# Kernel tuning notes

Hardware: AMD Instinct MI355X
Metric: run time of the kernel (lower is better)

The kernel has to match this reference:

```python
import jax, jax.numpy as jnp
import numpy as np

DIM = 1024; N_LAYERS = 4; N_HEADS = 16; HEAD_DIM = DIM // N_HEADS
HIDDEN = 2816; VOCAB = 256; EPS = 1e-5; THETA = 10000.0
B, S = 1, 2048


def _rmsnorm(x, w):
    xf = x.astype(jnp.float32)
    n = xf * jax.lax.rsqrt(jnp.mean(xf * xf, axis=-1, keepdims=True) + EPS)
    return n.astype(x.dtype) * w


def _rope(x, cos, sin):
    # x: [B,S,H,hd]; torch view_as_complex pairs consecutive elements (0,1),(2,3),...
    xr = x[..., 0::2].astype(jnp.float32)
    xi = x[..., 1::2].astype(jnp.float32)
    c = cos[None, :, None, :]
    s = sin[None, :, None, :]
    outr = xr * c - xi * s
    outi = xr * s + xi * c
    out = jnp.stack([outr, outi], axis=-1).reshape(x.shape)
    return out.astype(x.dtype)


def setup_inputs() -> dict:
    key = jax.random.key(0)
    ks = jax.random.split(key, 10)
    std = 0.02
    def w(k, shape):
        return jax.random.normal(k, shape, jnp.float32) * std
    return {
        "tokens": jax.random.randint(ks[0], (B, S), 0, VOCAB, dtype=jnp.int32),
        "tok_emb": w(ks[1], (VOCAB, DIM)),
        "wq": w(ks[2], (N_LAYERS, DIM, DIM)),
        "wk": w(ks[3], (N_LAYERS, DIM, DIM)),
        "wv": w(ks[4], (N_LAYERS, DIM, DIM)),
        "wo": w(ks[5], (N_LAYERS, DIM, DIM)),
        "w1": w(ks[6], (N_LAYERS, HIDDEN, DIM)),
        "w2": w(ks[7], (N_LAYERS, DIM, HIDDEN)),
        "w3": w(ks[8], (N_LAYERS, HIDDEN, DIM)),
        "attn_norm_w": jnp.ones((N_LAYERS, DIM), jnp.float32),
        "ffn_norm_w": jnp.ones((N_LAYERS, DIM), jnp.float32),
        "final_norm_w": jnp.ones((DIM,), jnp.float32),
        "out_w": w(ks[9], (VOCAB, DIM)),
    }


def reference(tokens, tok_emb, wq, wk, wv, wo, w1, w2, w3,
              attn_norm_w, ffn_norm_w, final_norm_w, out_w):
    seqlen = tokens.shape[1]
    # precompute_freqs_cis
    inv = 1.0 / (THETA ** (jnp.arange(0, HEAD_DIM, 2, dtype=jnp.float32) / HEAD_DIM))
    t = jnp.arange(seqlen, dtype=jnp.float32)
    freqs = jnp.outer(t, inv)          # [S, hd/2]
    cos, sin = jnp.cos(freqs), jnp.sin(freqs)
    scale = 1.0 / np.sqrt(HEAD_DIM)

    h = tok_emb[tokens]                # [B,S,D]

    def block(h, p):
        lwq, lwk, lwv, lwo, lw1, lw2, lw3, anw, fnw = p
        x = _rmsnorm(h, anw)
        q = (x @ lwq.T).reshape(B, seqlen, N_HEADS, HEAD_DIM)
        k = (x @ lwk.T).reshape(B, seqlen, N_HEADS, HEAD_DIM)
        v = (x @ lwv.T).reshape(B, seqlen, N_HEADS, HEAD_DIM)
        q = _rope(q, cos, sin)
        k = _rope(k, cos, sin)
        # non-causal full attention (eval mode: no diffusion mask, no dropout)
        scores = jnp.einsum('bqhd,bkhd->bhqk', q, k) * scale
        probs = jax.nn.softmax(scores, axis=-1)
        attn = jnp.einsum('bhqk,bkhd->bqhd', probs, v).reshape(B, seqlen, DIM)
        h = h + attn @ lwo.T
        x = _rmsnorm(h, fnw)
        ff = (jax.nn.silu(x @ lw1.T) * (x @ lw3.T)) @ lw2.T
        return h + ff, None

    h, _ = jax.lax.scan(block, h, (wq, wk, wv, wo, w1, w2, w3, attn_norm_w, ffn_norm_w))
    h = _rmsnorm(h, final_norm_w)
    # targets=None path: logits only for the last position
    return h[:, -1:, :] @ out_w.T      # [B,1,VOCAB]
```

## Files before the change

kernel.cpp:

```cpp
#include <hip/hip_runtime.h>
#include <stdint.h>

typedef __bf16 bf16;
typedef __bf16 bf16x4 __attribute__((ext_vector_type(4)));
typedef __bf16 bf16x8 __attribute__((ext_vector_type(8)));
typedef float f32x4 __attribute__((ext_vector_type(4)));
typedef float f32x16 __attribute__((ext_vector_type(16)));

#define SEQ 2048
#define DIM 1024
#define NHEAD 16
#define HDIM 64
#define HID 2816
#define NLAYER 4

__device__ __forceinline__ void gload_lds16(const void* g, void* l) {
  __builtin_amdgcn_global_load_lds(
      (const __attribute__((address_space(1))) void*)g,
      (__attribute__((address_space(3))) void*)l, 16, 0, 0);
}

template <int MODE, int BM, int BN>
__global__ __launch_bounds__(256) void gemm_bt(
    const bf16* __restrict__ A, const bf16* __restrict__ B,
    bf16* __restrict__ Cb, float* __restrict__ Cf, const float* R,
    int M, int N, int K)
{
  constexpr int MR = BM / 32;
  constexpr int NR = BN / 32;
  constexpr int LA = BM / 64;
  constexpr int LB = BN / 64;
  __shared__ bf16 As[2 * BM * 32];
  __shared__ bf16 Bs[2 * BN * 32];
  const int tid  = threadIdx.x;
  const int wv   = tid >> 6;
  const int lane = tid & 63;
  const int lo = lane & 15, hi = lane >> 4;
  const int row0 = blockIdx.y * BM;
  const int col0 = blockIdx.x * BN;
  const int wr = (wv >> 1) * (BM / 2);
  const int wc = (wv & 1) * (BN / 2);

  f32x4 acc[MR][NR];
  const f32x4 zero = {0.f, 0.f, 0.f, 0.f};
#pragma unroll
  for (int m = 0; m < MR; ++m)
#pragma unroll
    for (int n = 0; n < NR; ++n) acc[m][n] = zero;

  const bf16* ag = A + (size_t)(row0 + (tid >> 2)) * K + (tid & 3) * 8;
  const bf16* bg = B + (size_t)(col0 + (tid >> 2)) * K + (tid & 3) * 8;

  auto stage = [&](int buf, int k) {
#pragma unroll
    for (int i = 0; i < LA; ++i)
      gload_lds16(ag + k + (size_t)i*64*K, &As[buf*BM*32 + i*2048 + wv*512]);
#pragma unroll
    for (int i = 0; i < LB; ++i)
      gload_lds16(bg + k + (size_t)i*64*K, &Bs[buf*BN*32 + i*2048 + wv*512]);
  };
  auto compute = [&](int buf) {
    bf16x8 af[MR], bfv[NR];
#pragma unroll
    for (int m = 0; m < MR; ++m)
      af[m] = *(const bf16x8*)&As[buf*BM*32 + (wr + m*16 + lo)*32 + hi*8];
#pragma unroll
    for (int n = 0; n < NR; ++n)
      bfv[n] = *(const bf16x8*)&Bs[buf*BN*32 + (wc + n*16 + lo)*32 + hi*8];
#pragma unroll
    for (int m = 0; m < MR; ++m)
#pragma unroll
      for (int n = 0; n < NR; ++n)
        acc[m][n] = __builtin_amdgcn_mfma_f32_16x16x32_bf16(af[m], bfv[n], acc[m][n], 0, 0, 0);
  };

  stage(0, 0);
  __syncthreads();
  for (int k0 = 0; k0 < K; k0 += 64) {
    stage(1, k0 + 32);
    compute(0);
    __syncthreads();
    if (k0 + 64 < K) stage(0, k0 + 64);
    compute(1);
    __syncthreads();
  }

#pragma unroll
  for (int m = 0; m < MR; ++m)
#pragma unroll
    for (int n = 0; n < NR; ++n)
#pragma unroll
      for (int r = 0; r < 4; ++r) {
        const int row = row0 + wr + m * 16 + hi * 4 + r;
        const int col = col0 + wc + n * 16 + lo;
        const size_t idx = (size_t)row * N + col;
        if (MODE == 0) Cb[idx] = (bf16)acc[m][n][r];
        else           Cf[idx] = R[idx] + acc[m][n][r];
      }
}

__device__ __forceinline__ void softmax_pv(
    f32x16& s, float& m, float& lsum, f32x16& o0, f32x16& o1,
    const bf16x8 (&vf)[2][2], int h)
{
  float mx = s[0];
#pragma unroll
  for (int r = 1; r < 16; ++r) mx = fmaxf(mx, s[r]);
  mx = fmaxf(mx, __shfl_xor(mx, 32));
  if (!__all(mx <= m + 8.0f)) {
    float mnew = fmaxf(m, mx);
    float corr = __expf(m - mnew);
    m = mnew; lsum *= corr;
#pragma unroll
    for (int r = 0; r < 16; ++r) { o0[r] *= corr; o1[r] *= corr; }
  }
  float p[16]; float ps = 0.f;
#pragma unroll
  for (int r = 0; r < 16; ++r) { p[r] = __expf(s[r] - m); ps += p[r]; }
  ps += __shfl_xor(ps, 32);
  lsum += ps;

  unsigned int w[4][2];
#pragma unroll
  for (int g = 0; g < 4; ++g)
#pragma unroll
    for (int t2 = 0; t2 < 2; ++t2) {
      union { bf16 b[2]; unsigned int u; } pk;
      pk.b[0] = (bf16)p[g*4 + 2*t2];
      pk.b[1] = (bf16)p[g*4 + 2*t2 + 1];
      w[g][t2] = pk.u;
    }

#pragma unroll
  for (int c = 0; c < 2; ++c) {
    unsigned int keep0 = h ? w[2*c+1][0] : w[2*c][0];
    unsigned int keep1 = h ? w[2*c+1][1] : w[2*c][1];
    unsigned int send0 = h ? w[2*c][0]   : w[2*c+1][0];
    unsigned int send1 = h ? w[2*c][1]   : w[2*c+1][1];
    unsigned int r0 = __shfl_xor(send0, 32);
    unsigned int r1 = __shfl_xor(send1, 32);
    union { unsigned int u[4]; bf16x8 v; } pf;
    pf.u[0] = h ? r0 : keep0;
    pf.u[1] = h ? r1 : keep1;
    pf.u[2] = h ? keep0 : r0;
    pf.u[3] = h ? keep1 : r1;
    __builtin_amdgcn_s_setprio(1);
    o0 = __builtin_amdgcn_mfma_f32_32x32x16_bf16(vf[c][0], pf.v, o0, 0, 0, 0);
    o1 = __builtin_amdgcn_mfma_f32_32x32x16_bf16(vf[c][1], pf.v, o1, 0, 0, 0);
    __builtin_amdgcn_s_setprio(0);
  }
}

__device__ __forceinline__ void attn_tile64(
    const bf16* __restrict__ kb, const bf16* __restrict__ vb,
    const bf16x8 (&qfA)[4], const bf16x8 (&qfB)[4],
    bf16x8 (&kc)[4], bf16x8 (&kn)[4],
    f32x16& oA0, f32x16& oA1, f32x16& oB0, f32x16& oB1,
    float& mA, float& lA, float& mB, float& lB,
    int j0, int jn, int q5, int h)
{
  bf16x8 vf[2][2];
#pragma unroll
  for (int c = 0; c < 2; ++c)
#pragma unroll
    for (int dh = 0; dh < 2; ++dh)
      vf[c][dh] = *(const bf16x8*)&vb[(size_t)(dh*32 + q5)*2048 + j0 + c*16];
  {
    const bf16* kp = kb + (size_t)(jn + q5)*3072;
#pragma unroll
    for (int dc = 0; dc < 4; ++dc) kn[dc] = *(const bf16x8*)(kp + dc*16);
  }
  f32x16 sA, sB;
#pragma unroll
  for (int r = 0; r < 16; ++r) { sA[r] = 0.f; sB[r] = 0.f; }
  __builtin_amdgcn_s_setprio(1);
#pragma unroll
  for (int dc = 0; dc < 4; ++dc) {
    sA = __builtin_amdgcn_mfma_f32_32x32x16_bf16(kc[dc], qfA[dc], sA, 0, 0, 0);
    sB = __builtin_amdgcn_mfma_f32_32x32x16_bf16(kc[dc], qfB[dc], sB, 0, 0, 0);
  }
  __builtin_amdgcn_s_setprio(0);

  softmax_pv(sA, mA, lA, oA0, oA1, vf, h);
  softmax_pv(sB, mB, lB, oB0, oB1, vf, h);
}

__global__ __launch_bounds__(256, 2) void attn_kernel(const bf16* __restrict__ qkv,
    const bf16* __restrict__ vt, bf16* __restrict__ outb)
{
  __shared__ float Osh[4][32][65];
  __shared__ float msh[4][32];
  __shared__ float lsh[4][32];

  const int tid = threadIdx.x;
  const int wv = tid >> 6;
  const int lane = tid & 63;
  const int q5 = lane & 31, h = lane >> 5;
  const int hh = blockIdx.x;
  const int q0 = blockIdx.y * 64;

  bf16x8 qfA[4], qfB[4];
#pragma unroll
  for (int dc = 0; dc < 4; ++dc) {
    bf16x8 xa = *(const bf16x8*)&qkv[(size_t)(q0 + q5)*3072      + hh*64 + h*8 + dc*16];
    bf16x8 xb = *(const bf16x8*)&qkv[(size_t)(q0 + 32 + q5)*3072 + hh*64 + h*8 + dc*16];
#pragma unroll
    for (int j = 0; j < 8; ++j) {
      xa[j] = (bf16)(0.125f * (float)xa[j]);
      xb[j] = (bf16)(0.125f * (float)xb[j]);
    }
    qfA[dc] = xa; qfB[dc] = xb;
  }

  const bf16* kb = qkv + 1024 + hh*64 + h*8;
  const bf16* vb = vt + (size_t)hh*64*2048 + h*8;

  f32x16 oA0, oA1, oB0, oB1;
#pragma unroll
  for (int r = 0; r < 16; ++r) { oA0[r]=0.f; oA1[r]=0.f; oB0[r]=0.f; oB1[r]=0.f; }
  float mA = -1e30f, lA = 0.f, mB = -1e30f, lB = 0.f;

  bf16x8 ka[4], ka2[4];
  {
    const bf16* kp = kb + (size_t)(wv*32 + q5)*3072;
#pragma unroll
    for (int dc = 0; dc < 4; ++dc) ka[dc] = *(const bf16x8*)(kp + dc*16);
  }

  for (int t = 0; t < 16; t += 2) {
    attn_tile64(kb, vb, qfA, qfB, ka, ka2, oA0, oA1, oB0, oB1,
                mA, lA, mB, lB,
                (wv + 4*t)*32,     ((wv + 4*(t+1)) & 63)*32, q5, h);
    attn_tile64(kb, vb, qfA, qfB, ka2, ka, oA0, oA1, oB0, oB1,
                mA, lA, mB, lB,
                (wv + 4*(t+1))*32, ((wv + 4*(t+2)) & 63)*32, q5, h);
  }

  const int q = tid >> 3, d0 = (tid & 7) * 8;
#pragma unroll
  for (int pass = 0; pass < 2; ++pass) {
    const f32x16& p0 = pass ? oB0 : oA0;
    const f32x16& p1 = pass ? oB1 : oA1;
#pragma unroll
    for (int r = 0; r < 16; ++r) {
      const int dr = (r & 3) + 8*(r >> 2) + 4*h;
      Osh[wv][q5][dr]      = p0[r];
      Osh[wv][q5][32 + dr] = p1[r];
    }
    if (h == 0) {
      msh[wv][q5] = pass ? mB : mA;
      lsh[wv][q5] = pass ? lB : lA;
    }
    __syncthreads();
    {
      float mm = fmaxf(fmaxf(msh[0][q], msh[1][q]), fmaxf(msh[2][q], msh[3][q]));
      float e0 = __expf(msh[0][q] - mm), e1 = __expf(msh[1][q] - mm),
            e2 = __expf(msh[2][q] - mm), e3 = __expf(msh[3][q] - mm);
      float L = e0*lsh[0][q] + e1*lsh[1][q] + e2*lsh[2][q] + e3*lsh[3][q];
      float rinv = 1.0f / L;
      bf16x8 outv;
#pragma unroll
      for (int j = 0; j < 8; ++j) {
        float sum = e0*Osh[0][q][d0+j] + e1*Osh[1][q][d0+j]
                  + e2*Osh[2][q][d0+j] + e3*Osh[3][q][d0+j];
        outv[j] = (bf16)(sum * rinv);
      }
      *(bf16x8*)&outb[(size_t)(q0 + pass*32 + q)*DIM + hh*64 + d0] = outv;
    }
    __syncthreads();
  }
}

__global__ __launch_bounds__(256) void rope_init_kernel(float* __restrict__ ct, float* __restrict__ st) {
  int idx = blockIdx.x * 256 + threadIdx.x;
  if (idx >= SEQ * 32) return;
  int s = idx >> 5, i = idx & 31;
  float inv = powf(10000.0f, -(float)i / 32.0f);
  float f = (float)s * inv;
  ct[idx] = cosf(f);
  st[idx] = sinf(f);
}

__global__ __launch_bounds__(256) void cast_kernel(const float* __restrict__ src,
    bf16* __restrict__ dst, int perLayer, int dstStride, int dstOff, int L)
{
  int i = blockIdx.x * 256 + threadIdx.x;
  int e = i * 4;
  if (e >= perLayer * L) return;
  int l = e / perLayer;
  int o = e - l * perLayer;
  float4 v = *(const float4*)(src + e);
  bf16x4 b;
  b[0] = (bf16)v.x; b[1] = (bf16)v.y; b[2] = (bf16)v.z; b[3] = (bf16)v.w;
  *(bf16x4*)(dst + (size_t)l * dstStride + dstOff + o) = b;
}

__global__ __launch_bounds__(256) void embed_kernel(const int* __restrict__ tok,
    const float* __restrict__ emb, float* __restrict__ h)
{
  int s = blockIdx.x, t = threadIdx.x;
  int v = tok[s];
  ((float4*)(h + (size_t)s * DIM))[t] = ((const float4*)(emb + (size_t)v * DIM))[t];
}

__global__ __launch_bounds__(256) void rmsnorm_kernel(const float* __restrict__ h,
    const float* __restrict__ w, bf16* __restrict__ outb)
{
  int row = blockIdx.x, tid = threadIdx.x;
  float4 v = ((const float4*)(h + (size_t)row * DIM))[tid];
  float ss = v.x*v.x + v.y*v.y + v.z*v.z + v.w*v.w;
#pragma unroll
  for (int off = 1; off < 64; off <<= 1) ss += __shfl_xor(ss, off);
  __shared__ float red[4];
  if ((tid & 63) == 0) red[tid >> 6] = ss;
  __syncthreads();
  float tot = red[0] + red[1] + red[2] + red[3];
  float inv = rsqrtf(tot * (1.0f / DIM) + 1e-5f);
  float4 wv4 = ((const float4*)w)[tid];
  bf16x4 o;
  o[0] = (bf16)(v.x * inv * wv4.x);
  o[1] = (bf16)(v.y * inv * wv4.y);
  o[2] = (bf16)(v.z * inv * wv4.z);
  o[3] = (bf16)(v.w * inv * wv4.w);
  ((bf16x4*)(outb + (size_t)row * DIM))[tid] = o;
}

__global__ __launch_bounds__(256) void final_rms_kernel(const float* __restrict__ hrow,
    const float* __restrict__ w, float* __restrict__ fl)
{
  int tid = threadIdx.x;
  float4 v = ((const float4*)hrow)[tid];
  float ss = v.x*v.x + v.y*v.y + v.z*v.z + v.w*v.w;
#pragma unroll
  for (int off = 1; off < 64; off <<= 1) ss += __shfl_xor(ss, off);
  __shared__ float red[4];
  if ((tid & 63) == 0) red[tid >> 6] = ss;
  __syncthreads();
  float tot = red[0] + red[1] + red[2] + red[3];
  float inv = rsqrtf(tot * (1.0f / DIM) + 1e-5f);
  float4 wv4 = ((const float4*)w)[tid];
  float4 o;
  o.x = v.x * inv * wv4.x;
  o.y = v.y * inv * wv4.y;
  o.z = v.z * inv * wv4.z;
  o.w = v.w * inv * wv4.w;
  ((float4*)fl)[tid] = o;
}

__global__ __launch_bounds__(256) void rope_kernel(bf16* __restrict__ qkv,
    const float* __restrict__ ct, const float* __restrict__ st)
{
  int idx = blockIdx.x * 256 + threadIdx.x;
  if (idx >= SEQ * 128) return;
  int s = idx >> 7, rem = idx & 127;
  int h = rem >> 3, c8 = rem & 7;
  int d0 = c8 * 8, i0 = c8 * 4;
  float4 cv = *(const float4*)&ct[s*32 + i0];
  float4 sv = *(const float4*)&st[s*32 + i0];
  float c[4]  = {cv.x, cv.y, cv.z, cv.w};
  float sn[4] = {sv.x, sv.y, sv.z, sv.w};
  size_t base = (size_t)s * 3072 + h * 64 + d0;
#pragma unroll
  for (int part = 0; part < 2; ++part) {
    bf16x8 x = *(bf16x8*)&qkv[base + part * 1024];
    bf16x8 o;
#pragma unroll
    for (int p = 0; p < 4; ++p) {
      float xr = (float)x[2*p], xi = (float)x[2*p+1];
      o[2*p]   = (bf16)(xr * c[p] - xi * sn[p]);
      o[2*p+1] = (bf16)(xr * sn[p] + xi * c[p]);
    }
    *(bf16x8*)&qkv[base + part * 1024] = o;
  }
}

__global__ __launch_bounds__(256) void vtrans_kernel(const bf16* __restrict__ qkv,
    bf16* __restrict__ vt)
{
  int i = blockIdx.x * 256 + threadIdx.x;
  if (i >= SEQ * DIM) return;
  int d = i >> 11, j = i & 2047;
  vt[(size_t)d * SEQ + j] = qkv[(size_t)j * 3072 + 2048 + d];
}

__global__ __launch_bounds__(256) void silu_kernel(const bf16* __restrict__ ug,
    bf16* __restrict__ hb)
{
  int i = blockIdx.x * 256 + threadIdx.x;
  int s = i / 352, j8 = (i - s * 352) * 8;
  if (s >= SEQ) return;
  bf16x8 u = *(const bf16x8*)&ug[(size_t)s * 5632 + j8];
  bf16x8 g = *(const bf16x8*)&ug[(size_t)s * 5632 + 2816 + j8];
  bf16x8 o;
#pragma unroll
  for (int t = 0; t < 8; ++t) {
    float x = (float)u[t];
    float y = x / (1.f + __expf(-x)) * (float)g[t];
    o[t] = (bf16)y;
  }
  *(bf16x8*)&hb[(size_t)s * HID + j8] = o;
}

__global__ __launch_bounds__(64) void logits_kernel(const float* __restrict__ fl,
    const float* __restrict__ ow, float* __restrict__ outp)
{
  int v = blockIdx.x, lane = threadIdx.x;
  const float* row = ow + (size_t)v * DIM;
  float s = 0.f;
#pragma unroll
  for (int t = 0; t < 16; ++t) {
    int d = t * 64 + lane;
    s += fl[d] * row[d];
  }
#pragma unroll
  for (int off = 1; off < 64; off <<= 1) s += __shfl_xor(s, off);
  if (lane == 0) outp[v] = s;
}

extern "C" void kernel_launch(void* const* d_in, const int* in_sizes, int n_in,
                              void* d_out, int out_size, void* d_ws, size_t ws_size,
                              hipStream_t stream)
{
  const int*   tokens = (const int*)  d_in[0];
  const float* temb   = (const float*)d_in[1];
  const float* wq  = (const float*)d_in[2];
  const float* wk  = (const float*)d_in[3];
  const float* wvv = (const float*)d_in[4];
  const float* wo  = (const float*)d_in[5];
  const float* w1  = (const float*)d_in[6];
  const float* w2  = (const float*)d_in[7];
  const float* w3  = (const float*)d_in[8];
  const float* anw = (const float*)d_in[9];
  const float* fnw = (const float*)d_in[10];
  const float* finw= (const float*)d_in[11];
  const float* outw= (const float*)d_in[12];
  float* out = (float*)d_out;

  char* wsp = (char*)d_ws;
  size_t off = 0;
  auto take = [&](size_t bytes) -> void* {
    void* r = wsp + off;
    off += (bytes + 255) & ~(size_t)255;
    return r;
  };
  bf16* wqkv = (bf16*)take((size_t)NLAYER * 3072 * DIM * 2);
  bf16* wob  = (bf16*)take((size_t)NLAYER * DIM * DIM * 2);
  bf16* w13  = (bf16*)take((size_t)NLAYER * 2 * HID * DIM * 2);
  bf16* w2b  = (bf16*)take((size_t)NLAYER * DIM * HID * 2);
  float* h   = (float*)take((size_t)SEQ * DIM * 4);
  bf16* xn   = (bf16*)take((size_t)SEQ * DIM * 2);
  bf16* qkvb = (bf16*)take((size_t)SEQ * 3072 * 2);
  bf16* vtb  = (bf16*)take((size_t)DIM * SEQ * 2);
  bf16* attnb= (bf16*)take((size_t)SEQ * DIM * 2);
  bf16* ugb  = (bf16*)take((size_t)SEQ * 2 * HID * 2);
  bf16* hbb  = (bf16*)take((size_t)SEQ * HID * 2);
  float* ct  = (float*)take((size_t)SEQ * 32 * 4);
  float* st  = (float*)take((size_t)SEQ * 32 * 4);
  float* fl  = (float*)take((size_t)DIM * 4);

  rope_init_kernel<<<SEQ * 32 / 256, 256, 0, stream>>>(ct, st);

  const int PLd = DIM * DIM;
  const int PLh = HID * DIM;
  cast_kernel<<<PLd * NLAYER / 1024, 256, 0, stream>>>(wq,  wqkv, PLd, 3 * PLd, 0,       NLAYER);
  cast_kernel<<<PLd * NLAYER / 1024, 256, 0, stream>>>(wk,  wqkv, PLd, 3 * PLd, PLd,     NLAYER);
  cast_kernel<<<PLd * NLAYER / 1024, 256, 0, stream>>>(wvv, wqkv, PLd, 3 * PLd, 2 * PLd, NLAYER);
  cast_kernel<<<PLd * NLAYER / 1024, 256, 0, stream>>>(wo,  wob,  PLd, PLd,     0,       NLAYER);
  cast_kernel<<<PLh * NLAYER / 1024, 256, 0, stream>>>(w1,  w13,  PLh, 2 * PLh, 0,       NLAYER);
  cast_kernel<<<PLh * NLAYER / 1024, 256, 0, stream>>>(w3,  w13,  PLh, 2 * PLh, PLh,     NLAYER);
  cast_kernel<<<PLh * NLAYER / 1024, 256, 0, stream>>>(w2,  w2b,  PLh, PLh,     0,       NLAYER);

  embed_kernel<<<SEQ, 256, 0, stream>>>(tokens, temb, h);

  for (int l = 0; l < NLAYER; ++l) {
    const bf16* lwqkv = wqkv + (size_t)l * 3 * PLd;
    const bf16* lwo   = wob  + (size_t)l * PLd;
    const bf16* lw13  = w13  + (size_t)l * 2 * PLh;
    const bf16* lw2   = w2b  + (size_t)l * PLh;

    rmsnorm_kernel<<<SEQ, 256, 0, stream>>>(h, anw + l * DIM, xn);
    gemm_bt<0,128,128><<<dim3(24, 16), 256, 0, stream>>>(xn, lwqkv, qkvb, nullptr, nullptr, SEQ, 3072, DIM);
    rope_kernel<<<SEQ * 128 / 256, 256, 0, stream>>>(qkvb, ct, st);
    vtrans_kernel<<<SEQ * DIM / 256, 256, 0, stream>>>(qkvb, vtb);
    attn_kernel<<<dim3(16, 32), 256, 0, stream>>>(qkvb, vtb, attnb);
    gemm_bt<1,64,64><<<dim3(16, 32), 256, 0, stream>>>(attnb, lwo, nullptr, h, h, SEQ, DIM, DIM);
    rmsnorm_kernel<<<SEQ, 256, 0, stream>>>(h, fnw + l * DIM, xn);
    gemm_bt<0,128,128><<<dim3(44, 16), 256, 0, stream>>>(xn, lw13, ugb, nullptr, nullptr, SEQ, 2 * HID, DIM);
    silu_kernel<<<SEQ * HID / 8 / 256, 256, 0, stream>>>(ugb, hbb);
    gemm_bt<1,64,64><<<dim3(16, 32), 256, 0, stream>>>(hbb, lw2, nullptr, h, h, SEQ, DIM, HID);
  }

  final_rms_kernel<<<1, 256, 0, stream>>>(h + (size_t)(SEQ - 1) * DIM, finw, fl);
  logits_kernel<<<256, 64, 0, stream>>>(fl, outw, out);
}
```

Before: 793.2 us.

## Fuse SiLU-gate into W1/W3 GEMM epilogue and tile V transpose via LDS

Interleaves W1 and W3 rows in 16-row groups at cast time so each GEMM wave holds matching up and gate accumulators. The new MODE 2 epilogue then applies SiLU(u)*g and writes the hidden activation directly, removing the 2048x5632 intermediate buffer and the separate silu kernel. It also rewrites the V transpose to use a 64x64 shared-memory tile with vector loads and stores instead of strided scalar accesses. The fused path depends on the MFMA fragment mapping lining up with the 16-row interleave.

```diff
diff --git a/kernel.cpp b/kernel.cpp
--- a/kernel.cpp
+++ b/kernel.cpp
@@ -85,18 +85,34 @@
     __syncthreads();
   }
 
-#pragma unroll
-  for (int m = 0; m < MR; ++m)
-#pragma unroll
-    for (int n = 0; n < NR; ++n)
-#pragma unroll
-      for (int r = 0; r < 4; ++r) {
-        const int row = row0 + wr + m * 16 + hi * 4 + r;
-        const int col = col0 + wc + n * 16 + lo;
-        const size_t idx = (size_t)row * N + col;
-        if (MODE == 0) Cb[idx] = (bf16)acc[m][n][r];
-        else           Cf[idx] = R[idx] + acc[m][n][r];
-      }
+  if (MODE == 2) {
+    const int hstride = N >> 1;
+#pragma unroll
+    for (int m = 0; m < MR; ++m)
+#pragma unroll
+      for (int p = 0; p < NR/2; ++p)
+#pragma unroll
+        for (int r = 0; r < 4; ++r) {
+          const int row  = row0 + wr + m * 16 + hi * 4 + r;
+          const int hcol = (col0 + wc)/2 + p * 16 + lo;
+          float u = acc[m][2*p][r], g = acc[m][2*p+1][r];
+          float y = u / (1.f + __expf(-u)) * g;
+          Cb[(size_t)row * hstride + hcol] = (bf16)y;
+        }
+  } else {
+#pragma unroll
+    for (int m = 0; m < MR; ++m)
+#pragma unroll
+      for (int n = 0; n < NR; ++n)
+#pragma unroll
+        for (int r = 0; r < 4; ++r) {
+          const int row = row0 + wr + m * 16 + hi * 4 + r;
+          const int col = col0 + wc + n * 16 + lo;
+          const size_t idx = (size_t)row * N + col;
+          if (MODE == 0) Cb[idx] = (bf16)acc[m][n][r];
+          else           Cf[idx] = R[idx] + acc[m][n][r];
+        }
+  }
 }
 
 __device__ __forceinline__ void softmax_pv(
@@ -295,6 +311,23 @@
   *(bf16x4*)(dst + (size_t)l * dstStride + dstOff + o) = b;
 }
 
+__global__ __launch_bounds__(256) void cast_interleave_kernel(const float* __restrict__ src,
+    bf16* __restrict__ dst, int isW3)
+{
+  const int PLh = HID * DIM;
+  int i = blockIdx.x * 256 + threadIdx.x;
+  int e = i * 4;
+  if (e >= PLh * NLAYER) return;
+  int l = e / PLh;
+  int rem = e - l * PLh;
+  int r = rem >> 10, c = rem & 1023;
+  int dr = (r >> 4) * 32 + (isW3 ? 16 : 0) + (r & 15);
+  float4 v = *(const float4*)(src + e);
+  bf16x4 b;
+  b[0] = (bf16)v.x; b[1] = (bf16)v.y; b[2] = (bf16)v.z; b[3] = (bf16)v.w;
+  *(bf16x4*)(dst + (size_t)l * 2 * PLh + (size_t)dr * 1024 + c) = b;
+}
+
 __global__ __launch_bounds__(256) void embed_kernel(const int* __restrict__ tok,
     const float* __restrict__ emb, float* __restrict__ h)
 {
@@ -377,28 +410,35 @@
 __global__ __launch_bounds__(256) void vtrans_kernel(const bf16* __restrict__ qkv,
     bf16* __restrict__ vt)
 {
-  int i = blockIdx.x * 256 + threadIdx.x;
-  if (i >= SEQ * DIM) return;
-  int d = i >> 11, j = i & 2047;
-  vt[(size_t)d * SEQ + j] = qkv[(size_t)j * 3072 + 2048 + d];
-}
-
-__global__ __launch_bounds__(256) void silu_kernel(const bf16* __restrict__ ug,
-    bf16* __restrict__ hb)
-{
-  int i = blockIdx.x * 256 + threadIdx.x;
-  int s = i / 352, j8 = (i - s * 352) * 8;
-  if (s >= SEQ) return;
-  bf16x8 u = *(const bf16x8*)&ug[(size_t)s * 5632 + j8];
-  bf16x8 g = *(const bf16x8*)&ug[(size_t)s * 5632 + 2816 + j8];
-  bf16x8 o;
-#pragma unroll
-  for (int t = 0; t < 8; ++t) {
-    float x = (float)u[t];
-    float y = x / (1.f + __expf(-x)) * (float)g[t];
-    o[t] = (bf16)y;
-  }
-  *(bf16x8*)&hb[(size_t)s * HID + j8] = o;
+  __shared__ unsigned short T[64][66];
+  const int tj = blockIdx.x & 31;
+  const int td = blockIdx.x >> 5;
+  const int t = threadIdx.x;
+  {
+    const int j = t >> 2, d0 = (t & 3) * 16;
+    const bf16* src = qkv + (size_t)(tj*64 + j)*3072 + 2048 + td*64 + d0;
+    bf16x8 a = *(const bf16x8*)src;
+    bf16x8 b = *(const bf16x8*)(src + 8);
+    union { bf16 v; unsigned short u; } cv;
+#pragma unroll
+    for (int i = 0; i < 8; ++i) {
+      cv.v = a[i]; T[j][d0 + i] = cv.u;
+      cv.v = b[i]; T[j][d0 + 8 + i] = cv.u;
+    }
+  }
+  __syncthreads();
+  {
+    const int d = t >> 2, j0 = (t & 3) * 16;
+    union { bf16x8 v; unsigned short u[8]; } oa, ob;
+#pragma unroll
+    for (int i = 0; i < 8; ++i) {
+      oa.u[i] = T[j0 + i][d];
+      ob.u[i] = T[j0 + 8 + i][d];
+    }
+    bf16* dst = vt + (size_t)(td*64 + d)*2048 + tj*64 + j0;
+    *(bf16x8*)dst = oa.v;
+    *(bf16x8*)(dst + 8) = ob.v;
+  }
 }
 
 __global__ __launch_bounds__(64) void logits_kernel(const float* __restrict__ fl,
@@ -452,7 +492,6 @@
   bf16* qkvb = (bf16*)take((size_t)SEQ * 3072 * 2);
   bf16* vtb  = (bf16*)take((size_t)DIM * SEQ * 2);
   bf16* attnb= (bf16*)take((size_t)SEQ * DIM * 2);
-  bf16* ugb  = (bf16*)take((size_t)SEQ * 2 * HID * 2);
   bf16* hbb  = (bf16*)take((size_t)SEQ * HID * 2);
   float* ct  = (float*)take((size_t)SEQ * 32 * 4);
   float* st  = (float*)take((size_t)SEQ * 32 * 4);
@@ -466,8 +505,8 @@
   cast_kernel<<<PLd * NLAYER / 1024, 256, 0, stream>>>(wk,  wqkv, PLd, 3 * PLd, PLd,     NLAYER);
   cast_kernel<<<PLd * NLAYER / 1024, 256, 0, stream>>>(wvv, wqkv, PLd, 3 * PLd, 2 * PLd, NLAYER);
   cast_kernel<<<PLd * NLAYER / 1024, 256, 0, stream>>>(wo,  wob,  PLd, PLd,     0,       NLAYER);
-  cast_kernel<<<PLh * NLAYER / 1024, 256, 0, stream>>>(w1,  w13,  PLh, 2 * PLh, 0,       NLAYER);
-  cast_kernel<<<PLh * NLAYER / 1024, 256, 0, stream>>>(w3,  w13,  PLh, 2 * PLh, PLh,     NLAYER);
+  cast_interleave_kernel<<<PLh * NLAYER / 1024, 256, 0, stream>>>(w1, w13, 0);
+  cast_interleave_kernel<<<PLh * NLAYER / 1024, 256, 0, stream>>>(w3, w13, 1);
   cast_kernel<<<PLh * NLAYER / 1024, 256, 0, stream>>>(w2,  w2b,  PLh, PLh,     0,       NLAYER);
 
   embed_kernel<<<SEQ, 256, 0, stream>>>(tokens, temb, h);
@@ -481,12 +520,11 @@
     rmsnorm_kernel<<<SEQ, 256, 0, stream>>>(h, anw + l * DIM, xn);
     gemm_bt<0,128,128><<<dim3(24, 16), 256, 0, stream>>>(xn, lwqkv, qkvb, nullptr, nullptr, SEQ, 3072, DIM);
     rope_kernel<<<SEQ * 128 / 256, 256, 0, stream>>>(qkvb, ct, st);
-    vtrans_kernel<<<SEQ * DIM / 256, 256, 0, stream>>>(qkvb, vtb);
+    vtrans_kernel<<<512, 256, 0, stream>>>(qkvb, vtb);
     attn_kernel<<<dim3(16, 32), 256, 0, stream>>>(qkvb, vtb, attnb);
     gemm_bt<1,64,64><<<dim3(16, 32), 256, 0, stream>>>(attnb, lwo, nullptr, h, h, SEQ, DIM, DIM);
     rmsnorm_kernel<<<SEQ, 256, 0, stream>>>(h, fnw + l * DIM, xn);
-    gemm_bt<0,128,128><<<dim3(44, 16), 256, 0, stream>>>(xn, lw13, ugb, nullptr, nullptr, SEQ, 2 * HID, DIM);
-    silu_kernel<<<SEQ * HID / 8 / 256, 256, 0, stream>>>(ugb, hbb);
+    gemm_bt<2,128,128><<<dim3(44, 16), 256, 0, stream>>>(xn, lw13, hbb, nullptr, nullptr, SEQ, 2 * HID, DIM);
     gemm_bt<1,64,64><<<dim3(16, 32), 256, 0, stream>>>(hbb, lw2, nullptr, h, h, SEQ, DIM, HID);
   }
 
```

New measurement: 730.9 us. -7.9%, faster.
